# Kernel tuning notes

Measured on AMD Instinct MI355X. Metric: run time of the kernel, lower is better.

## Reference

```python
import jax, jax.numpy as jnp
import numpy as np

N_NODES = 100000
N_EDGES = 800000
D = 64
N_ITERS = 3  # n_layers - 1


def setup_inputs() -> dict:
    key = jax.random.key(0)
    k1, k2, k3, k4 = jax.random.split(key, 4)
    x = jax.random.normal(k1, (N_NODES, D), dtype=jnp.float32)
    edge_index = jax.random.randint(k2, (2, N_EDGES), 0, N_NODES, dtype=jnp.int64)
    edge_weight = jax.random.uniform(k3, (N_EDGES,), dtype=jnp.float32)
    # Linear(64, 64) weight, scaled ~ kaiming so 3 stacked layers stay bounded
    W = jax.random.normal(k4, (D, D), dtype=jnp.float32) * (1.0 / np.sqrt(D))
    b = jnp.zeros((D,), dtype=jnp.float32)
    return {"x": x, "edge_index": edge_index, "edge_weight": edge_weight, "W": W, "b": b}


def reference(x, edge_index, edge_weight, W, b):
    # Faithful math of RPINetEncoder.forward: (n_layers-1) iterations of
    # LinearAggregation (weighted scatter-add message passing + shared Linear)
    # followed by ReLU. Dropout output is discarded in the original -> no-op.
    src = edge_index[0]
    dst = edge_index[1]
    n = x.shape[0]
    for _ in range(N_ITERS):
        msgs = edge_weight[:, None] * x[src]                      # [E, D] gather
        agg = jax.ops.segment_sum(msgs, dst, num_segments=n)      # [N, D] scatter-add
        x = jax.nn.relu(agg @ W.T + b)                            # shared linear + relu
    return x
```

## Files before the change

### kernel.cpp

```cpp
#include <hip/hip_runtime.h>
#include <hip/hip_bf16.h>

#define D 64
#define FP_SCALE 262144.0f
#define FP_INV   (1.0f / 262144.0f)

__device__ __forceinline__ unsigned short f2bf(float f) {
    unsigned int u = __float_as_uint(f);
    u += 0x7fffu + ((u >> 16) & 1u);
    return (unsigned short)(u >> 16);
}

__global__ void hist_kernel(const int* __restrict__ dst, int* __restrict__ counts, int E) {
    int e = blockIdx.x * blockDim.x + threadIdx.x;
    if (e < E) atomicAdd(&counts[dst[e]], 1);
}

__global__ void alloc_kernel(int* __restrict__ counts_cursor, int2* __restrict__ seg,
                             int* __restrict__ total, int N) {
    int n = blockIdx.x * blockDim.x + threadIdx.x;
    int lane = threadIdx.x & 63;
    int c = (n < N) ? counts_cursor[n] : 0;
    int incl = c;
    #pragma unroll
    for (int off = 1; off < 64; off <<= 1) {
        int t = __shfl_up(incl, off);
        if (lane >= off) incl += t;
    }
    int wsum = __shfl(incl, 63);
    int base = 0;
    if (lane == 63) base = atomicAdd(total, wsum);
    base = __shfl(base, 63);
    if (n < N) {
        int st = base + incl - c;
        seg[n] = make_int2(st, c);
        counts_cursor[n] = st;
    }
}

__global__ void fill_kernel(const int* __restrict__ src, const int* __restrict__ dst,
                            const float* __restrict__ ew, int* __restrict__ cursor,
                            float2* __restrict__ perm, int E) {
    int e = blockIdx.x * blockDim.x + threadIdx.x;
    if (e < E) {
        int p = atomicAdd(&cursor[dst[e]], 1);
        perm[p] = make_float2(__int_as_float(src[e]), ew[e] * FP_SCALE);
    }
}

__global__ void cvt_kernel(const float* __restrict__ in, unsigned short* __restrict__ out, int n4) {
    int i = blockIdx.x * blockDim.x + threadIdx.x;
    if (i >= n4) return;
    float4 v = reinterpret_cast<const float4*>(in)[i];
    ushort4 o;
    o.x = f2bf(v.x); o.y = f2bf(v.y); o.z = f2bf(v.z); o.w = f2bf(v.w);
    reinterpret_cast<ushort4*>(out)[i] = o;
}

#define EDGE_ACC(m)                                                        \
    {                                                                      \
        int s_ = __float_as_int((m).x);                                    \
        float w_ = (m).y;                                                  \
        uint2 u_ = *reinterpret_cast<const uint2*>(&xb[(size_t)s_ * D + c]); \
        ix += (int)(w_ * __uint_as_float(u_.x << 16));                     \
        iy += (int)(w_ * __uint_as_float(u_.x & 0xffff0000u));             \
        iz += (int)(w_ * __uint_as_float(u_.y << 16));                     \
        iw += (int)(w_ * __uint_as_float(u_.y & 0xffff0000u));             \
    }

template<bool OUT_BF>
__global__ void gather_linear_kernel(const unsigned short* __restrict__ xb,
                                     const float2* __restrict__ perm,
                                     const int2* __restrict__ seg,
                                     const float* __restrict__ W,
                                     const float* __restrict__ bias,
                                     void* __restrict__ xout, int N) {
    __shared__ float aggRow[4][D];
    int t = threadIdx.x;
    int wave = t >> 6;
    int lane = t & 63;

    float4 wreg[16];
    #pragma unroll
    for (int q = 0; q < 16; ++q)
        wreg[q] = *reinterpret_cast<const float4*>(&W[(size_t)lane * D + 4 * q]);
    float blane = bias[lane];

    int g = lane >> 4;
    int c = (lane & 15) << 2;
    int nwaves = gridDim.x * 4;
    for (int n = blockIdx.x * 4 + wave; n < N; n += nwaves) {
        int2 sc = seg[n];
        int st = sc.x, cnt = sc.y;
        int ix = 0, iy = 0, iz = 0, iw = 0;
        int k = g;
        for (; k + 12 < cnt; k += 16) {
            float2 m0 = perm[st + k];
            float2 m1 = perm[st + k + 4];
            float2 m2 = perm[st + k + 8];
            float2 m3 = perm[st + k + 12];
            EDGE_ACC(m0); EDGE_ACC(m1); EDGE_ACC(m2); EDGE_ACC(m3);
        }
        for (; k < cnt; k += 4) {
            float2 m0 = perm[st + k];
            EDGE_ACC(m0);
        }
        #pragma unroll
        for (int mask = 16; mask <= 32; mask <<= 1) {
            ix += __shfl_xor(ix, mask);
            iy += __shfl_xor(iy, mask);
            iz += __shfl_xor(iz, mask);
            iw += __shfl_xor(iw, mask);
        }
        if (g == 0) {
            *reinterpret_cast<float4*>(&aggRow[wave][c]) =
                make_float4((float)ix * FP_INV, (float)iy * FP_INV,
                            (float)iz * FP_INV, (float)iw * FP_INV);
        }
        float o0 = 0.f, o1 = 0.f, o2 = 0.f, o3 = 0.f;
        #pragma unroll
        for (int q = 0; q < 16; ++q) {
            float4 a = *reinterpret_cast<const float4*>(&aggRow[wave][4 * q]);
            o0 = fmaf(a.x, wreg[q].x, o0);
            o1 = fmaf(a.y, wreg[q].y, o1);
            o2 = fmaf(a.z, wreg[q].z, o2);
            o3 = fmaf(a.w, wreg[q].w, o3);
        }
        float o = fmaxf(blane + ((o0 + o1) + (o2 + o3)), 0.0f);
        if (OUT_BF) ((unsigned short*)xout)[(size_t)n * D + lane] = f2bf(o);
        else        ((float*)xout)[(size_t)n * D + lane] = o;
    }
}

__global__ void rpi_scatter_kernel(const float* __restrict__ x,
                                   const int* __restrict__ src,
                                   const int* __restrict__ dst,
                                   const float* __restrict__ ew,
                                   int* __restrict__ agg, int E) {
    int tid = blockIdx.x * blockDim.x + threadIdx.x;
    int e = tid >> 4;
    if (e >= E) return;
    int c = (tid & 15) << 2;
    int s = src[e], d = dst[e];
    float w = ew[e] * FP_SCALE;
    float4 v = *reinterpret_cast<const float4*>(&x[(size_t)s * D + c]);
    int* o = &agg[(size_t)d * D + c];
    atomicAdd(o + 0, (int)(w * v.x));
    atomicAdd(o + 1, (int)(w * v.y));
    atomicAdd(o + 2, (int)(w * v.z));
    atomicAdd(o + 3, (int)(w * v.w));
}

__global__ void rpi_linear_relu_kernel(const int* __restrict__ agg,
                                       const float* __restrict__ W,
                                       const float* __restrict__ b,
                                       float* __restrict__ out, int N) {
    __shared__ float Ws[D][D + 1];
    __shared__ float bs[D];
    int t = threadIdx.x;
    for (int i = t; i < D * D; i += 256) Ws[i >> 6][i & 63] = W[i];
    if (t < D) bs[t] = b[t];
    __syncthreads();
    int wave = t >> 6, lane = t & 63;
    int nwaves = gridDim.x * 4;
    for (int n = blockIdx.x * 4 + wave; n < N; n += nwaves) {
        const int* arow = &agg[(size_t)n * D];
        float acc = bs[lane];
        #pragma unroll
        for (int d = 0; d < D; ++d) acc = fmaf((float)arow[d] * FP_INV, Ws[lane][d], acc);
        out[(size_t)n * D + lane] = fmaxf(acc, 0.0f);
    }
}

extern "C" void kernel_launch(void* const* d_in, const int* in_sizes, int n_in,
                              void* d_out, int out_size, void* d_ws, size_t ws_size,
                              hipStream_t stream) {
    const float* x0 = (const float*)d_in[0];
    const int*   ei = (const int*)d_in[1];
    const float* ew = (const float*)d_in[2];
    const float* W  = (const float*)d_in[3];
    const float* b  = (const float*)d_in[4];
    float* out = (float*)d_out;

    int N = in_sizes[0] / D;
    int E = in_sizes[2];
    const int* src = ei;
    const int* dst = ei + E;

    size_t xeb      = (size_t)N * D * sizeof(unsigned short);
    size_t intBytes = ((size_t)3 * N + 4) * sizeof(int);
    size_t need     = 2 * xeb + intBytes + (size_t)E * sizeof(float2);

    if (ws_size >= need) {
        unsigned short* xb1 = (unsigned short*)d_ws;
        unsigned short* xb2 = xb1 + (size_t)N * D;
        int2*  seg    = (int2*)((char*)d_ws + 2 * xeb);
        int*   cursor = (int*)(seg + N);
        int*   total  = cursor + N;
        float2* perm  = (float2*)((char*)d_ws + 2 * xeb + intBytes);

        hipMemsetAsync(cursor, 0, (size_t)(N + 2) * sizeof(int), stream);
        int eb = (E + 255) / 256;
        int nb = (N + 255) / 256;
        int n4 = N * D / 4;
        hist_kernel <<<eb, 256, 0, stream>>>(dst, cursor, E);
        alloc_kernel<<<nb, 256, 0, stream>>>(cursor, seg, total, N);
        fill_kernel <<<eb, 256, 0, stream>>>(src, dst, ew, cursor, perm, E);
        cvt_kernel  <<<(n4 + 255) / 256, 256, 0, stream>>>(x0, xb1, n4);

        gather_linear_kernel<true> <<<4096, 256, 0, stream>>>(xb1, perm, seg, W, b, xb2, N);
        gather_linear_kernel<true> <<<4096, 256, 0, stream>>>(xb2, perm, seg, W, b, xb1, N);
        gather_linear_kernel<false><<<4096, 256, 0, stream>>>(xb1, perm, seg, W, b, out, N);
    } else {
        int* agg = (int*)d_ws;
        const float* xcur = x0;
        int sb = (E * 16 + 255) / 256;
        for (int it = 0; it < 3; ++it) {
            hipMemsetAsync(agg, 0, (size_t)N * D * sizeof(int), stream);
            rpi_scatter_kernel<<<sb, 256, 0, stream>>>(xcur, src, dst, ew, agg, E);
            rpi_linear_relu_kernel<<<2048, 256, 0, stream>>>(agg, W, b, out, N);
            xcur = out;
        }
    }
}
```

Before: 376.6 us.

## Split gather-linear into edge-chunked LDS aggregation plus separate linear kernel

Replaces the per-node CSR gather fused with the linear layer by an edge-balanced aggregation kernel. It processes fixed 512-edge chunks of the dst-sorted edge list, accumulates into LDS slots with shared atomics, and flushes to a global int accumulator (interior nodes stored directly, boundary nodes via atomics). A separate linear+ReLU kernel then reads that accumulator. The segment allocation also becomes a deterministic three-pass scan instead of atomic wave bases. This targets load imbalance from uneven node degrees, but it adds a full N×D int round trip through global memory, memsets and extra launches per layer.

```diff
diff --git a/kernel.cpp b/kernel.cpp
--- a/kernel.cpp
+++ b/kernel.cpp
@@ -4,6 +4,8 @@
 #define D 64
 #define FP_SCALE 262144.0f
 #define FP_INV   (1.0f / 262144.0f)
+#define CHUNK 512
+#define SLOTS 128
 
 __device__ __forceinline__ unsigned short f2bf(float f) {
     unsigned int u = __float_as_uint(f);
@@ -16,35 +18,75 @@
     if (e < E) atomicAdd(&counts[dst[e]], 1);
 }
 
-__global__ void alloc_kernel(int* __restrict__ counts_cursor, int2* __restrict__ seg,
-                             int* __restrict__ total, int N) {
-    int n = blockIdx.x * blockDim.x + threadIdx.x;
-    int lane = threadIdx.x & 63;
-    int c = (n < N) ? counts_cursor[n] : 0;
+__global__ void part_kernel(const int* __restrict__ counts, int* __restrict__ partial, int N) {
+    __shared__ int ws4[4];
+    int t = threadIdx.x, lane = t & 63, w = t >> 6;
+    int n = blockIdx.x * 256 + t;
+    int c = (n < N) ? counts[n] : 0;
+    #pragma unroll
+    for (int off = 32; off > 0; off >>= 1) c += __shfl_down(c, off);
+    if (lane == 0) ws4[w] = c;
+    __syncthreads();
+    if (t == 0) partial[blockIdx.x] = ws4[0] + ws4[1] + ws4[2] + ws4[3];
+}
+
+__global__ void scan_kernel(int* __restrict__ partial, int nb) {
+    __shared__ int wsum[8];
+    int t = threadIdx.x, lane = t & 63, w = t >> 6;
+    int carry = 0;
+    for (int base = 0; base < nb; base += 512) {
+        int i = base + t;
+        int v = (i < nb) ? partial[i] : 0;
+        int incl = v;
+        #pragma unroll
+        for (int off = 1; off < 64; off <<= 1) {
+            int x = __shfl_up(incl, off);
+            if (lane >= off) incl += x;
+        }
+        if (lane == 63) wsum[w] = incl;
+        __syncthreads();
+        int wpre = 0;
+        for (int j = 0; j < w; ++j) wpre += wsum[j];
+        int tot = 0;
+        for (int j = 0; j < 8; ++j) tot += wsum[j];
+        if (i < nb) partial[i] = carry + wpre + incl - v;
+        carry += tot;
+        __syncthreads();
+    }
+}
+
+__global__ void seg_kernel(const int* __restrict__ counts, const int* __restrict__ partial,
+                           int2* __restrict__ seg, int* __restrict__ cursor, int N) {
+    __shared__ int ws4[4];
+    int t = threadIdx.x, lane = t & 63, w = t >> 6;
+    int n = blockIdx.x * 256 + t;
+    int c = (n < N) ? counts[n] : 0;
     int incl = c;
     #pragma unroll
     for (int off = 1; off < 64; off <<= 1) {
-        int t = __shfl_up(incl, off);
-        if (lane >= off) incl += t;
-    }
-    int wsum = __shfl(incl, 63);
-    int base = 0;
-    if (lane == 63) base = atomicAdd(total, wsum);
-    base = __shfl(base, 63);
+        int x = __shfl_up(incl, off);
+        if (lane >= off) incl += x;
+    }
+    if (lane == 63) ws4[w] = incl;
+    __syncthreads();
+    int wpre = 0;
+    for (int j = 0; j < w; ++j) wpre += ws4[j];
+    int st = partial[blockIdx.x] + wpre + incl - c;
     if (n < N) {
-        int st = base + incl - c;
         seg[n] = make_int2(st, c);
-        counts_cursor[n] = st;
+        cursor[n] = st;
     }
 }
 
 __global__ void fill_kernel(const int* __restrict__ src, const int* __restrict__ dst,
                             const float* __restrict__ ew, int* __restrict__ cursor,
-                            float2* __restrict__ perm, int E) {
+                            float2* __restrict__ perm, int* __restrict__ permDst, int E) {
     int e = blockIdx.x * blockDim.x + threadIdx.x;
     if (e < E) {
-        int p = atomicAdd(&cursor[dst[e]], 1);
+        int d = dst[e];
+        int p = atomicAdd(&cursor[d], 1);
         perm[p] = make_float2(__int_as_float(src[e]), ew[e] * FP_SCALE);
+        permDst[p] = d;
     }
 }
 
@@ -57,76 +99,88 @@
     reinterpret_cast<ushort4*>(out)[i] = o;
 }
 
-#define EDGE_ACC(m)                                                        \
-    {                                                                      \
-        int s_ = __float_as_int((m).x);                                    \
-        float w_ = (m).y;                                                  \
-        uint2 u_ = *reinterpret_cast<const uint2*>(&xb[(size_t)s_ * D + c]); \
-        ix += (int)(w_ * __uint_as_float(u_.x << 16));                     \
-        iy += (int)(w_ * __uint_as_float(u_.x & 0xffff0000u));             \
-        iz += (int)(w_ * __uint_as_float(u_.y << 16));                     \
-        iw += (int)(w_ * __uint_as_float(u_.y & 0xffff0000u));             \
-    }
+__global__ void agg_kernel(const unsigned short* __restrict__ xb,
+                           const float2* __restrict__ perm,
+                           const int* __restrict__ permDst,
+                           const int2* __restrict__ seg,
+                           int* __restrict__ agg, int E) {
+    __shared__ int acc[SLOTS * D];
+    int t = threadIdx.x;
+    int base = blockIdx.x * CHUNK;
+    int end = min(base + CHUNK, E);
+    int slotBase = permDst[base];
+    int span = permDst[end - 1] - slotBase + 1;
+    int zspan = min(span, SLOTS);
+    for (int i = t; i < zspan * D; i += 256) acc[i] = 0;
+    __syncthreads();
+
+    int g = t >> 4;
+    int c = (t & 15) << 2;
+    for (int e = base + g; e < end; e += 16) {
+        int dn = permDst[e];
+        float2 m = perm[e];
+        int s = __float_as_int(m.x);
+        float w = m.y;
+        uint2 u = *reinterpret_cast<const uint2*>(&xb[(size_t)s * D + c]);
+        int v0 = (int)(w * __uint_as_float(u.x << 16));
+        int v1 = (int)(w * __uint_as_float(u.x & 0xffff0000u));
+        int v2 = (int)(w * __uint_as_float(u.y << 16));
+        int v3 = (int)(w * __uint_as_float(u.y & 0xffff0000u));
+        int slot = dn - slotBase;
+        if (slot < SLOTS) {
+            atomicAdd(&acc[slot * D + c + 0], v0);
+            atomicAdd(&acc[slot * D + c + 1], v1);
+            atomicAdd(&acc[slot * D + c + 2], v2);
+            atomicAdd(&acc[slot * D + c + 3], v3);
+        } else {
+            size_t o = (size_t)dn * D + c;
+            atomicAdd(&agg[o + 0], v0);
+            atomicAdd(&agg[o + 1], v1);
+            atomicAdd(&agg[o + 2], v2);
+            atomicAdd(&agg[o + 3], v3);
+        }
+    }
+    __syncthreads();
+
+    int wave = t >> 6, lane = t & 63;
+    for (int s = wave; s < zspan; s += 4) {
+        int node = slotBase + s;
+        int2 sg = seg[node];
+        int v = acc[s * D + lane];
+        bool interior = (sg.x >= base) && (sg.x + sg.y <= end);
+        size_t o = (size_t)node * D + lane;
+        if (interior) agg[o] = v;
+        else if (v) atomicAdd(&agg[o], v);
+    }
+}
 
 template<bool OUT_BF>
-__global__ void gather_linear_kernel(const unsigned short* __restrict__ xb,
-                                     const float2* __restrict__ perm,
-                                     const int2* __restrict__ seg,
-                                     const float* __restrict__ W,
-                                     const float* __restrict__ bias,
-                                     void* __restrict__ xout, int N) {
-    __shared__ float aggRow[4][D];
-    int t = threadIdx.x;
-    int wave = t >> 6;
-    int lane = t & 63;
-
+__launch_bounds__(256, 4)
+__global__ void linear_kernel(const int* __restrict__ agg,
+                              const float* __restrict__ W,
+                              const float* __restrict__ bias,
+                              void* __restrict__ xout, int N) {
+    __shared__ float rowSh[4][D];
+    int t = threadIdx.x, wave = t >> 6, lane = t & 63;
     float4 wreg[16];
     #pragma unroll
     for (int q = 0; q < 16; ++q)
         wreg[q] = *reinterpret_cast<const float4*>(&W[(size_t)lane * D + 4 * q]);
-    float blane = bias[lane];
-
-    int g = lane >> 4;
-    int c = (lane & 15) << 2;
+    float bl = bias[lane];
     int nwaves = gridDim.x * 4;
     for (int n = blockIdx.x * 4 + wave; n < N; n += nwaves) {
-        int2 sc = seg[n];
-        int st = sc.x, cnt = sc.y;
-        int ix = 0, iy = 0, iz = 0, iw = 0;
-        int k = g;
-        for (; k + 12 < cnt; k += 16) {
-            float2 m0 = perm[st + k];
-            float2 m1 = perm[st + k + 4];
-            float2 m2 = perm[st + k + 8];
-            float2 m3 = perm[st + k + 12];
-            EDGE_ACC(m0); EDGE_ACC(m1); EDGE_ACC(m2); EDGE_ACC(m3);
-        }
-        for (; k < cnt; k += 4) {
-            float2 m0 = perm[st + k];
-            EDGE_ACC(m0);
-        }
-        #pragma unroll
-        for (int mask = 16; mask <= 32; mask <<= 1) {
-            ix += __shfl_xor(ix, mask);
-            iy += __shfl_xor(iy, mask);
-            iz += __shfl_xor(iz, mask);
-            iw += __shfl_xor(iw, mask);
-        }
-        if (g == 0) {
-            *reinterpret_cast<float4*>(&aggRow[wave][c]) =
-                make_float4((float)ix * FP_INV, (float)iy * FP_INV,
-                            (float)iz * FP_INV, (float)iw * FP_INV);
-        }
+        int v = agg[(size_t)n * D + lane];
+        rowSh[wave][lane] = (float)v * FP_INV;
         float o0 = 0.f, o1 = 0.f, o2 = 0.f, o3 = 0.f;
         #pragma unroll
         for (int q = 0; q < 16; ++q) {
-            float4 a = *reinterpret_cast<const float4*>(&aggRow[wave][4 * q]);
+            float4 a = *reinterpret_cast<const float4*>(&rowSh[wave][4 * q]);
             o0 = fmaf(a.x, wreg[q].x, o0);
             o1 = fmaf(a.y, wreg[q].y, o1);
             o2 = fmaf(a.z, wreg[q].z, o2);
             o3 = fmaf(a.w, wreg[q].w, o3);
         }
-        float o = fmaxf(blane + ((o0 + o1) + (o2 + o3)), 0.0f);
+        float o = fmaxf(bl + ((o0 + o1) + (o2 + o3)), 0.0f);
         if (OUT_BF) ((unsigned short*)xout)[(size_t)n * D + lane] = f2bf(o);
         else        ((float*)xout)[(size_t)n * D + lane] = o;
     }
@@ -187,30 +241,49 @@
     const int* src = ei;
     const int* dst = ei + E;
 
-    size_t xeb      = (size_t)N * D * sizeof(unsigned short);
-    size_t intBytes = ((size_t)3 * N + 4) * sizeof(int);
-    size_t need     = 2 * xeb + intBytes + (size_t)E * sizeof(float2);
+    int nb = (N + 255) / 256;
+    size_t xeb = (size_t)N * D * sizeof(unsigned short);
+    size_t off = 0;
+    size_t o_xb1  = off; off += xeb;
+    size_t o_xb2  = off; off += xeb;
+    size_t o_perm = off; off += (size_t)E * sizeof(float2);
+    size_t o_pdst = off; off += (size_t)E * sizeof(int);
+    size_t o_seg  = off; off += (size_t)N * sizeof(int2);
+    size_t o_cnt  = off; off += (size_t)N * sizeof(int);
+    size_t o_part = off; off += ((size_t)nb + 16) * sizeof(int);
+    size_t need = off;
 
     if (ws_size >= need) {
-        unsigned short* xb1 = (unsigned short*)d_ws;
-        unsigned short* xb2 = xb1 + (size_t)N * D;
-        int2*  seg    = (int2*)((char*)d_ws + 2 * xeb);
-        int*   cursor = (int*)(seg + N);
-        int*   total  = cursor + N;
-        float2* perm  = (float2*)((char*)d_ws + 2 * xeb + intBytes);
-
-        hipMemsetAsync(cursor, 0, (size_t)(N + 2) * sizeof(int), stream);
+        unsigned short* xb1 = (unsigned short*)((char*)d_ws + o_xb1);
+        unsigned short* xb2 = (unsigned short*)((char*)d_ws + o_xb2);
+        float2* perm    = (float2*)((char*)d_ws + o_perm);
+        int*    permDst = (int*)((char*)d_ws + o_pdst);
+        int2*   seg     = (int2*)((char*)d_ws + o_seg);
+        int*    cnt_cur = (int*)((char*)d_ws + o_cnt);
+        int*    partial = (int*)((char*)d_ws + o_part);
+        int*    agg     = (int*)d_out;
+
         int eb = (E + 255) / 256;
-        int nb = (N + 255) / 256;
         int n4 = N * D / 4;
-        hist_kernel <<<eb, 256, 0, stream>>>(dst, cursor, E);
-        alloc_kernel<<<nb, 256, 0, stream>>>(cursor, seg, total, N);
-        fill_kernel <<<eb, 256, 0, stream>>>(src, dst, ew, cursor, perm, E);
-        cvt_kernel  <<<(n4 + 255) / 256, 256, 0, stream>>>(x0, xb1, n4);
-
-        gather_linear_kernel<true> <<<4096, 256, 0, stream>>>(xb1, perm, seg, W, b, xb2, N);
-        gather_linear_kernel<true> <<<4096, 256, 0, stream>>>(xb2, perm, seg, W, b, xb1, N);
-        gather_linear_kernel<false><<<4096, 256, 0, stream>>>(xb1, perm, seg, W, b, out, N);
+        int ab = (E + CHUNK - 1) / CHUNK;
+
+        hipMemsetAsync(cnt_cur, 0, (size_t)N * sizeof(int), stream);
+        hist_kernel<<<eb, 256, 0, stream>>>(dst, cnt_cur, E);
+        part_kernel<<<nb, 256, 0, stream>>>(cnt_cur, partial, N);
+        scan_kernel<<<1, 512, 0, stream>>>(partial, nb);
+        seg_kernel <<<nb, 256, 0, stream>>>(cnt_cur, partial, seg, cnt_cur, N);
+        fill_kernel<<<eb, 256, 0, stream>>>(src, dst, ew, cnt_cur, perm, permDst, E);
+        cvt_kernel <<<(n4 + 255) / 256, 256, 0, stream>>>(x0, xb1, n4);
+
+        hipMemsetAsync(agg, 0, (size_t)N * D * sizeof(int), stream);
+        agg_kernel<<<ab, 256, 0, stream>>>(xb1, perm, permDst, seg, agg, E);
+        linear_kernel<true><<<2048, 256, 0, stream>>>(agg, W, b, xb2, N);
+        hipMemsetAsync(agg, 0, (size_t)N * D * sizeof(int), stream);
+        agg_kernel<<<ab, 256, 0, stream>>>(xb2, perm, permDst, seg, agg, E);
+        linear_kernel<true><<<2048, 256, 0, stream>>>(agg, W, b, xb1, N);
+        hipMemsetAsync(agg, 0, (size_t)N * D * sizeof(int), stream);
+        agg_kernel<<<ab, 256, 0, stream>>>(xb1, perm, permDst, seg, agg, E);
+        linear_kernel<false><<<2048, 256, 0, stream>>>(agg, W, b, out, N);
     } else {
         int* agg = (int*)d_ws;
         const float* xcur = x0;
```

Result: slower. 468.1 us (+24.3%).
